# Kernel optimization log

Hardware: AMD Instinct MI355X
Metric: run time of the kernel (lower is better)

Reference implementation:

```python
import jax, jax.numpy as jnp
import numpy as np

E = 3_200_000
D = 16
N = 100_000


def setup_inputs() -> dict:
    key = jax.random.key(0)
    k1, k2 = jax.random.split(key)
    x = jax.random.normal(k1, (E, D), dtype=jnp.float32)
    edge_dst = jax.random.randint(k2, (E,), 0, N, dtype=jnp.int64)
    return {"x": x, "edge_dst": edge_dst, "num_nodes": N}


def reference(x, edge_dst, num_nodes):
    # sum_over_neighbours: scatter-add edge features to destination atoms -> [N, D]
    summed = jax.ops.segment_sum(x, edge_dst, num_segments=num_nodes)
    # number_of_neighbours(include_central_atom=True): per-atom edge count + 1
    counts = jax.ops.segment_sum(
        jnp.ones((x.shape[0],), dtype=x.dtype), edge_dst, num_segments=num_nodes
    ) + jnp.asarray(1.0, dtype=x.dtype)
    # left_aligned_div by sqrt(counts): broadcast counts over trailing feature dims
    return summed / jnp.sqrt(counts)[:, None]
```

## Files before the change

### kernel.cpp

```cpp
#include <hip/hip_runtime.h>

#define DFEAT 16
#define NPB 64
#define NPB_SHIFT 6
#define EB 8192
#define EB_SHIFT 13
#define BIN_THREADS 1024
#define SCAN_BLOCKS 256
#define SCAN_THREADS 256
#define SORT_CAP 4096

__global__ void na_bin_kernel(const int* __restrict__ edge_dst,
                              int* __restrict__ hist,
                              int E, int B, int nblocks) {
    extern __shared__ int h[];
    const int b = blockIdx.x;
    const int t = threadIdx.x;
    for (int i = t; i < B; i += BIN_THREADS) h[i] = 0;
    __syncthreads();
    const int base = b * EB;
    #pragma unroll
    for (int j = 0; j < EB / BIN_THREADS; ++j) {
        int e = base + j * BIN_THREADS + t;
        if (e < E) atomicAdd(&h[edge_dst[e] >> NPB_SHIFT], 1);
    }
    __syncthreads();
    for (int i = t; i < B; i += BIN_THREADS)
        hist[(size_t)i * nblocks + b] = h[i];
}

__global__ void na_scan_partials(const int* __restrict__ data,
                                 int* __restrict__ blockSums, int M) {
    __shared__ int lds[SCAN_THREADS];
    const int b = blockIdx.x, t = threadIdx.x;
    const int chb = (M + SCAN_BLOCKS - 1) / SCAN_BLOCKS;
    const int bbeg = b * chb;
    const int bend = min(bbeg + chb, M);
    const int cht = (chb + SCAN_THREADS - 1) / SCAN_THREADS;
    const int beg = min(bbeg + t * cht, bend);
    const int end = min(beg + cht, bend);
    int s = 0;
    for (int i = beg; i < end; ++i) s += data[i];
    lds[t] = s;
    __syncthreads();
    for (int off = SCAN_THREADS / 2; off > 0; off >>= 1) {
        if (t < off) lds[t] += lds[t + off];
        __syncthreads();
    }
    if (t == 0) blockSums[b] = lds[0];
}

__global__ void na_scan_blocksums(const int* __restrict__ blockSums,
                                  int* __restrict__ blockOffs) {
    __shared__ int lds[SCAN_BLOCKS];
    const int t = threadIdx.x;
    int v = blockSums[t];
    lds[t] = v;
    __syncthreads();
    for (int off = 1; off < SCAN_BLOCKS; off <<= 1) {
        int add = (t >= off) ? lds[t - off] : 0;
        __syncthreads();
        lds[t] += add;
        __syncthreads();
    }
    blockOffs[t] = lds[t] - v;
}

__global__ void na_scan_final(int* __restrict__ data,
                              const int* __restrict__ blockOffs, int M) {
    __shared__ int lds[SCAN_THREADS];
    const int b = blockIdx.x, t = threadIdx.x;
    const int chb = (M + SCAN_BLOCKS - 1) / SCAN_BLOCKS;
    const int bbeg = b * chb;
    const int bend = min(bbeg + chb, M);
    const int cht = (chb + SCAN_THREADS - 1) / SCAN_THREADS;
    const int beg = min(bbeg + t * cht, bend);
    const int end = min(beg + cht, bend);
    int s = 0;
    for (int i = beg; i < end; ++i) s += data[i];
    lds[t] = s;
    __syncthreads();
    for (int off = 1; off < SCAN_THREADS; off <<= 1) {
        int add = (t >= off) ? lds[t - off] : 0;
        __syncthreads();
        lds[t] += add;
        __syncthreads();
    }
    int run = blockOffs[b] + lds[t] - s;
    for (int i = beg; i < end; ++i) {
        int c = data[i];
        data[i] = run;
        run += c;
    }
}

__global__ void na_scatter_fused(const int* __restrict__ edge_dst,
                                 const int* __restrict__ offs,
                                 int* __restrict__ binned,
                                 int E, int B, int nblocks) {
    extern __shared__ int h[];
    const int b = blockIdx.x;
    const int t = threadIdx.x;
    for (int i = t; i < B; i += BIN_THREADS)
        h[i] = offs[(size_t)i * nblocks + b];
    __syncthreads();
    const int base = b * EB;
    #pragma unroll
    for (int j = 0; j < EB / BIN_THREADS; ++j) {
        int e = base + j * BIN_THREADS + t;
        if (e < E) {
            int n = edge_dst[e];
            int pos = atomicAdd(&h[n >> NPB_SHIFT], 1);
            binned[pos] = ((n & (NPB - 1)) << 22) | e;
        }
    }
}

__global__ __launch_bounds__(256, 4)
void na_sort_gather(const float* __restrict__ x,
                    const int* __restrict__ binned,
                    const int* __restrict__ offs,
                    float* __restrict__ out,
                    int E, int N, int B, int nblocks) {
    __shared__ int buf[SORT_CAP];
    __shared__ int sorted[SORT_CAP];
    __shared__ int cnt[NPB];
    __shared__ int cur[NPB];
    __shared__ int excl[NPB + 1];

    const int k = blockIdx.x;
    const int t = threadIdx.x;

    const int beg = offs[(size_t)k * nblocks];
    const int end = (k + 1 < B) ? offs[(size_t)(k + 1) * nblocks] : E;
    const int sz = end - beg;

    if (t < NPB) { cnt[t] = 0; cur[t] = 0; }
    __syncthreads();

    if (sz <= SORT_CAP) {
        for (int j = t; j < sz; j += 256) {
            int v = binned[beg + j];
            buf[j] = v;
            atomicAdd(&cnt[v >> 22], 1);
        }
        __syncthreads();
        if (t < 64) {
            int v = cnt[t];
            int inc = v;
            #pragma unroll
            for (int d = 1; d < 64; d <<= 1) {
                int u = __shfl_up(inc, d);
                if (t >= d) inc += u;
            }
            excl[t] = inc - v;
            if (t == 63) excl[NPB] = inc;
        }
        __syncthreads();
        for (int j = t; j < sz; j += 256) {
            int v = buf[j];
            int d = v >> 22;
            int r = atomicAdd(&cur[d], 1);
            sorted[excl[d] + r] = v & 0x3FFFFF;
        }
        __syncthreads();

        const int ln = t >> 2;
        const int q = t & 3;
        const float4* x4 = reinterpret_cast<const float4*>(x);

        const int lbeg = excl[ln], lend = excl[ln + 1];
        float ax = 0.f, ay = 0.f, az = 0.f, aw = 0.f;

        int i = lbeg;
        for (; i + 8 <= lend; i += 8) {
            int e0 = sorted[i + 0], e1 = sorted[i + 1];
            int e2 = sorted[i + 2], e3 = sorted[i + 3];
            int e4 = sorted[i + 4], e5 = sorted[i + 5];
            int e6 = sorted[i + 6], e7 = sorted[i + 7];
            float4 v0 = x4[(size_t)e0 * 4 + q];
            float4 v1 = x4[(size_t)e1 * 4 + q];
            float4 v2 = x4[(size_t)e2 * 4 + q];
            float4 v3 = x4[(size_t)e3 * 4 + q];
            float4 v4 = x4[(size_t)e4 * 4 + q];
            float4 v5 = x4[(size_t)e5 * 4 + q];
            float4 v6 = x4[(size_t)e6 * 4 + q];
            float4 v7 = x4[(size_t)e7 * 4 + q];
            ax += ((v0.x + v1.x) + (v2.x + v3.x)) + ((v4.x + v5.x) + (v6.x + v7.x));
            ay += ((v0.y + v1.y) + (v2.y + v3.y)) + ((v4.y + v5.y) + (v6.y + v7.y));
            az += ((v0.z + v1.z) + (v2.z + v3.z)) + ((v4.z + v5.z) + (v6.z + v7.z));
            aw += ((v0.w + v1.w) + (v2.w + v3.w)) + ((v4.w + v5.w) + (v6.w + v7.w));
        }
        for (; i < lend; ++i) {
            int e0 = sorted[i];
            float4 v0 = x4[(size_t)e0 * 4 + q];
            ax += v0.x; ay += v0.y; az += v0.z; aw += v0.w;
        }

        int n = k * NPB + ln;
        if (n < N) {
            float s = rsqrtf((float)(lend - lbeg) + 1.0f);
            float4 r; r.x = ax * s; r.y = ay * s; r.z = az * s; r.w = aw * s;
            reinterpret_cast<float4*>(out)[(size_t)n * 4 + q] = r;
        }
    } else {
        const int ln = t >> 2;
        const int q = t & 3;
        const float4* x4 = reinterpret_cast<const float4*>(x);
        int n = k * NPB + ln;
        if (n < N) {
            float ax = 0.f, ay = 0.f, az = 0.f, aw = 0.f;
            int deg = 0;
            for (int j = 0; j < sz; ++j) {
                int v = binned[beg + j];
                if ((v >> 22) == ln) {
                    float4 vv = x4[(size_t)(v & 0x3FFFFF) * 4 + q];
                    ax += vv.x; ay += vv.y; az += vv.z; aw += vv.w;
                    ++deg;
                }
            }
            float s = rsqrtf((float)deg + 1.0f);
            float4 r; r.x = ax * s; r.y = ay * s; r.z = az * s; r.w = aw * s;
            reinterpret_cast<float4*>(out)[(size_t)n * 4 + q] = r;
        }
    }
}

extern "C" void kernel_launch(void* const* d_in, const int* in_sizes, int n_in,
                              void* d_out, int out_size, void* d_ws, size_t ws_size,
                              hipStream_t stream) {
    const float* x        = (const float*)d_in[0];
    const int*   edge_dst = (const int*)d_in[1];
    float*       out      = (float*)d_out;

    const int E = in_sizes[1];
    const int N = out_size / DFEAT;
    const int B = (N + NPB - 1) >> NPB_SHIFT;
    const int nblocks = (E + EB - 1) >> EB_SHIFT;
    const int M = B * nblocks;

    int* binned    = (int*)d_ws;
    int* hist      = binned + E;
    int* blockSums = hist + M;
    int* blockOffs = blockSums + SCAN_BLOCKS;

    na_bin_kernel<<<nblocks, BIN_THREADS, B * sizeof(int), stream>>>(
        edge_dst, hist, E, B, nblocks);
    na_scan_partials<<<SCAN_BLOCKS, SCAN_THREADS, 0, stream>>>(hist, blockSums, M);
    na_scan_blocksums<<<1, SCAN_BLOCKS, 0, stream>>>(blockSums, blockOffs);
    na_scan_final<<<SCAN_BLOCKS, SCAN_THREADS, 0, stream>>>(hist, blockOffs, M);
    na_scatter_fused<<<nblocks, BIN_THREADS, B * sizeof(int), stream>>>(
        edge_dst, hist, binned, E, B, nblocks);
    na_sort_gather<<<B, 256, 0, stream>>>(x, binned, hist, out, E, N, B, nblocks);
}
```

Before: 130.7 us.

## Shrink sort LDS, raise occupancy, and split node gathers across 16-lane groups

The sort-gather kernel drops its LDS staging buffer and re-reads binned entries from global memory instead. It also lowers SORT_CAP and raises the launch-bounds occupancy target, so more blocks can be resident at once. The gather now uses 16 threads per node, which stride over edges in four slices and combine partial sums with xor shuffles, spreading uneven degrees more evenly. The bin and scatter kernels first batch all edge_dst loads into registers before doing their LDS atomics. The trade-offs are an extra global read of binned, more bins falling to the slow fallback path, and the shuffle overhead.

Result: no change. 129.7 us (-0.8%).

```diff
diff --git a/kernel.cpp b/kernel.cpp
--- a/kernel.cpp
+++ b/kernel.cpp
@@ -6,9 +6,10 @@
 #define EB 8192
 #define EB_SHIFT 13
 #define BIN_THREADS 1024
+#define BATCH (EB / BIN_THREADS)
 #define SCAN_BLOCKS 256
 #define SCAN_THREADS 256
-#define SORT_CAP 4096
+#define SORT_CAP 3072
 
 __global__ void na_bin_kernel(const int* __restrict__ edge_dst,
                               int* __restrict__ hist,
@@ -19,11 +20,17 @@
     for (int i = t; i < B; i += BIN_THREADS) h[i] = 0;
     __syncthreads();
     const int base = b * EB;
-    #pragma unroll
-    for (int j = 0; j < EB / BIN_THREADS; ++j) {
-        int e = base + j * BIN_THREADS + t;
-        if (e < E) atomicAdd(&h[edge_dst[e] >> NPB_SHIFT], 1);
-    }
+
+    int d[BATCH];
+    #pragma unroll
+    for (int jj = 0; jj < BATCH; ++jj) {
+        int e = base + jj * BIN_THREADS + t;
+        d[jj] = (e < E) ? edge_dst[e] : -1;
+    }
+    #pragma unroll
+    for (int jj = 0; jj < BATCH; ++jj)
+        if (d[jj] >= 0) atomicAdd(&h[d[jj] >> NPB_SHIFT], 1);
+
     __syncthreads();
     for (int i = t; i < B; i += BIN_THREADS)
         hist[(size_t)i * nblocks + b] = h[i];
@@ -105,24 +112,30 @@
         h[i] = offs[(size_t)i * nblocks + b];
     __syncthreads();
     const int base = b * EB;
-    #pragma unroll
-    for (int j = 0; j < EB / BIN_THREADS; ++j) {
-        int e = base + j * BIN_THREADS + t;
-        if (e < E) {
-            int n = edge_dst[e];
+
+    int d[BATCH];
+    #pragma unroll
+    for (int jj = 0; jj < BATCH; ++jj) {
+        int e = base + jj * BIN_THREADS + t;
+        d[jj] = (e < E) ? edge_dst[e] : -1;
+    }
+    #pragma unroll
+    for (int jj = 0; jj < BATCH; ++jj) {
+        if (d[jj] >= 0) {
+            int n = d[jj];
+            int e = base + jj * BIN_THREADS + t;
             int pos = atomicAdd(&h[n >> NPB_SHIFT], 1);
             binned[pos] = ((n & (NPB - 1)) << 22) | e;
         }
     }
 }
 
-__global__ __launch_bounds__(256, 4)
+__global__ __launch_bounds__(256, 7)
 void na_sort_gather(const float* __restrict__ x,
                     const int* __restrict__ binned,
                     const int* __restrict__ offs,
                     float* __restrict__ out,
                     int E, int N, int B, int nblocks) {
-    __shared__ int buf[SORT_CAP];
     __shared__ int sorted[SORT_CAP];
     __shared__ int cnt[NPB];
     __shared__ int cur[NPB];
@@ -139,11 +152,8 @@
     __syncthreads();
 
     if (sz <= SORT_CAP) {
-        for (int j = t; j < sz; j += 256) {
-            int v = binned[beg + j];
-            buf[j] = v;
-            atomicAdd(&cnt[v >> 22], 1);
-        }
+        for (int j = t; j < sz; j += 256)
+            atomicAdd(&cnt[binned[beg + j] >> 22], 1);
         __syncthreads();
         if (t < 64) {
             int v = cnt[t];
@@ -158,50 +168,56 @@
         }
         __syncthreads();
         for (int j = t; j < sz; j += 256) {
-            int v = buf[j];
+            int v = binned[beg + j];
             int d = v >> 22;
             int r = atomicAdd(&cur[d], 1);
             sorted[excl[d] + r] = v & 0x3FFFFF;
         }
         __syncthreads();
 
-        const int ln = t >> 2;
-        const int q = t & 3;
+        const int g = t >> 4;
+        const int lane16 = t & 15;
+        const int es = lane16 >> 2;
+        const int q = lane16 & 3;
         const float4* x4 = reinterpret_cast<const float4*>(x);
 
-        const int lbeg = excl[ln], lend = excl[ln + 1];
-        float ax = 0.f, ay = 0.f, az = 0.f, aw = 0.f;
-
-        int i = lbeg;
-        for (; i + 8 <= lend; i += 8) {
-            int e0 = sorted[i + 0], e1 = sorted[i + 1];
-            int e2 = sorted[i + 2], e3 = sorted[i + 3];
-            int e4 = sorted[i + 4], e5 = sorted[i + 5];
-            int e6 = sorted[i + 6], e7 = sorted[i + 7];
-            float4 v0 = x4[(size_t)e0 * 4 + q];
-            float4 v1 = x4[(size_t)e1 * 4 + q];
-            float4 v2 = x4[(size_t)e2 * 4 + q];
-            float4 v3 = x4[(size_t)e3 * 4 + q];
-            float4 v4 = x4[(size_t)e4 * 4 + q];
-            float4 v5 = x4[(size_t)e5 * 4 + q];
-            float4 v6 = x4[(size_t)e6 * 4 + q];
-            float4 v7 = x4[(size_t)e7 * 4 + q];
-            ax += ((v0.x + v1.x) + (v2.x + v3.x)) + ((v4.x + v5.x) + (v6.x + v7.x));
-            ay += ((v0.y + v1.y) + (v2.y + v3.y)) + ((v4.y + v5.y) + (v6.y + v7.y));
-            az += ((v0.z + v1.z) + (v2.z + v3.z)) + ((v4.z + v5.z) + (v6.z + v7.z));
-            aw += ((v0.w + v1.w) + (v2.w + v3.w)) + ((v4.w + v5.w) + (v6.w + v7.w));
-        }
-        for (; i < lend; ++i) {
-            int e0 = sorted[i];
-            float4 v0 = x4[(size_t)e0 * 4 + q];
-            ax += v0.x; ay += v0.y; az += v0.z; aw += v0.w;
-        }
-
-        int n = k * NPB + ln;
-        if (n < N) {
+        for (int ln = g; ln < NPB; ln += 16) {
+            int n = k * NPB + ln;
+            if (n >= N) break;
+            int lbeg = excl[ln], lend = excl[ln + 1];
+            float ax = 0.f, ay = 0.f, az = 0.f, aw = 0.f;
+
+            int i = lbeg + es;
+            for (; i + 12 < lend; i += 16) {
+                int e0 = sorted[i];
+                int e1 = sorted[i + 4];
+                int e2 = sorted[i + 8];
+                int e3 = sorted[i + 12];
+                float4 v0 = x4[(size_t)e0 * 4 + q];
+                float4 v1 = x4[(size_t)e1 * 4 + q];
+                float4 v2 = x4[(size_t)e2 * 4 + q];
+                float4 v3 = x4[(size_t)e3 * 4 + q];
+                ax += (v0.x + v1.x) + (v2.x + v3.x);
+                ay += (v0.y + v1.y) + (v2.y + v3.y);
+                az += (v0.z + v1.z) + (v2.z + v3.z);
+                aw += (v0.w + v1.w) + (v2.w + v3.w);
+            }
+            for (; i < lend; i += 4) {
+                int e0 = sorted[i];
+                float4 v0 = x4[(size_t)e0 * 4 + q];
+                ax += v0.x; ay += v0.y; az += v0.z; aw += v0.w;
+            }
+
+            ax += __shfl_xor(ax, 4); ay += __shfl_xor(ay, 4);
+            az += __shfl_xor(az, 4); aw += __shfl_xor(aw, 4);
+            ax += __shfl_xor(ax, 8); ay += __shfl_xor(ay, 8);
+            az += __shfl_xor(az, 8); aw += __shfl_xor(aw, 8);
+
             float s = rsqrtf((float)(lend - lbeg) + 1.0f);
-            float4 r; r.x = ax * s; r.y = ay * s; r.z = az * s; r.w = aw * s;
-            reinterpret_cast<float4*>(out)[(size_t)n * 4 + q] = r;
+            if (es == 0) {
+                float4 r; r.x = ax * s; r.y = ay * s; r.z = az * s; r.w = aw * s;
+                reinterpret_cast<float4*>(out)[(size_t)n * 4 + q] = r;
+            }
         }
     } else {
         const int ln = t >> 2;
```
